# Performance work log

Hardware: AMD Instinct MI355X
Metric: run time of the kernel (lower is better)

The kernel has to match this reference:

```python
import jax, jax.numpy as jnp
import numpy as np

D_MODEL = 1024
NHEAD = 16
HEAD_DIM = D_MODEL // NHEAD
ROPE_BASE = 10000.0


def rope_cos_sin(seq_len, dim, dtype=jnp.float32):
    inv_freq = 1.0 / (ROPE_BASE ** (jnp.arange(0, dim, 2, dtype=jnp.float32) / dim))
    t = jnp.arange(seq_len, dtype=jnp.float32)
    freqs = jnp.einsum('i,j->ij', t, inv_freq)        # [S, dim/2]
    emb = jnp.concatenate([freqs, freqs], axis=-1)    # [S, dim]
    return emb.astype(dtype), jnp.cos(emb).astype(dtype), jnp.sin(emb).astype(dtype)


def rotate_half(x):
    x1, x2 = jnp.split(x, 2, axis=-1)
    return jnp.concatenate([-x2, x1], axis=-1)


def setup_inputs() -> dict:
    key = jax.random.key(0)
    ks = jax.random.split(key, 11)
    B, S, D = 2, 2048, D_MODEL
    std = 1.0 / np.sqrt(D)
    return {
        'query': jax.random.normal(ks[0], (B, S, D), jnp.float32),
        'key_': jax.random.normal(ks[1], (B, S, D), jnp.float32),
        'value': jax.random.normal(ks[2], (B, S, D), jnp.float32),
        'Wq': jax.random.uniform(ks[3], (D, D), jnp.float32, -std, std),
        'bq': jax.random.uniform(ks[4], (D,), jnp.float32, -std, std),
        'Wk': jax.random.uniform(ks[5], (D, D), jnp.float32, -std, std),
        'bk': jax.random.uniform(ks[6], (D,), jnp.float32, -std, std),
        'Wv': jax.random.uniform(ks[7], (D, D), jnp.float32, -std, std),
        'bv': jax.random.uniform(ks[8], (D,), jnp.float32, -std, std),
        'Wo': jax.random.uniform(ks[9], (D, D), jnp.float32, -std, std),
        'bo': jax.random.uniform(ks[10], (D,), jnp.float32, -std, std),
    }


def reference(query, key_, value, Wq, bq, Wk, bk, Wv, bv, Wo, bo):
    B, T, D = query.shape
    S = key_.shape[1]
    H, Hd = NHEAD, HEAD_DIM
    scale = Hd ** -0.5
    # projections (torch Linear: x @ W^T + b), reshape to [B, H, L, Hd]
    q = (query @ Wq.T + bq).reshape(B, T, H, Hd).transpose(0, 2, 1, 3)
    k = (key_ @ Wk.T + bk).reshape(B, S, H, Hd).transpose(0, 2, 1, 3)
    v = (value @ Wv.T + bv).reshape(B, S, H, Hd).transpose(0, 2, 1, 3)
    # RoPE
    _, cos, sin = rope_cos_sin(max(T, S), Hd, query.dtype)
    cos_q, sin_q = cos[:T][None, None], sin[:S][None, None]
    q = q * cos_q + rotate_half(q) * sin_q
    k = k * cos_q + rotate_half(k) * sin_q
    # attention
    scores = jnp.einsum('bhtd,bhsd->bhts', q, k) * scale
    attn = jax.nn.softmax(scores, axis=-1)
    out = jnp.einsum('bhts,bhsd->bhtd', attn, v)
    out = out.transpose(0, 2, 1, 3).reshape(B, T, D)
    return out @ Wo.T + bo
```

## Files before the change

kernel.cpp:

```cpp
#include <hip/hip_runtime.h>
#include <hip/hip_bf16.h>
#include <math.h>

using bf16x8 = __attribute__((ext_vector_type(8))) short;
using f32x4  = __attribute__((ext_vector_type(4))) float;
using f32x16 = __attribute__((ext_vector_type(16))) float;

#define MFMA16(a,b,c) __builtin_amdgcn_mfma_f32_16x16x32_bf16(a,b,c,0,0,0)
#define MFMA32(a,b,c) __builtin_amdgcn_mfma_f32_32x32x16_bf16(a,b,c,0,0,0)

#define GLOAD_LDS16(g, s) __builtin_amdgcn_global_load_lds( \
    (const __attribute__((address_space(1))) unsigned int*)(const void*)(g), \
    (__attribute__((address_space(3))) unsigned int*)(void*)(s), 16, 0, 0)

static __device__ __forceinline__ short f2bf(float f) {
    __hip_bfloat16 h = __float2bfloat16(f);
    return *reinterpret_cast<short*>(&h);
}

static __device__ __forceinline__ int cvtpk(float lo, float hi) {
    int r;
    asm volatile("v_cvt_pk_bf16_f32 %0, %1, %2" : "=v"(r) : "v"(lo), "v"(hi));
    return r;
}

__global__ void prep_cast(const float* q, const float* k, const float* v,
                          const float* wq, const float* wk, const float* wv, const float* wo,
                          short* xq, short* xk, short* xv,
                          short* bwq, short* bwk, short* bwv, short* bwo) {
    const long NBIG = 1L << 20;
    const long NW   = 1L << 18;
    const long total = 3*NBIG + 4*NW;
    for (long i = (long)blockIdx.x*blockDim.x + threadIdx.x; i < total; i += (long)gridDim.x*blockDim.x) {
        const float* src; short* dst; long j = i;
        if (j < NBIG)              { src = q;  dst = xq;  }
        else if ((j -= NBIG) < NBIG) { src = k;  dst = xk;  }
        else if ((j -= NBIG) < NBIG) { src = v;  dst = xv;  }
        else if ((j -= NBIG) < NW)   { src = wq; dst = bwq; }
        else if ((j -= NW) < NW)     { src = wk; dst = bwk; }
        else if ((j -= NW) < NW)     { src = wv; dst = bwv; }
        else { j -= NW;              src = wo; dst = bwo; }
        float4 f = reinterpret_cast<const float4*>(src)[j];
        ushort4 o;
        o.x = (ushort)f2bf(f.x); o.y = (ushort)f2bf(f.y);
        o.z = (ushort)f2bf(f.z); o.w = (ushort)f2bf(f.w);
        reinterpret_cast<ushort4*>(dst)[j] = o;
    }
}

__global__ void rope_table(float* cost, float* sint) {
    int i = blockIdx.x*blockDim.x + threadIdx.x;
    int s = i >> 5, j = i & 31;
    double inv = pow(10000.0, -(double)j / 32.0);
    double a = (double)s * inv;
    cost[i] = (float)cos(a);
    sint[i] = (float)sin(a);
}

__device__ __forceinline__ void gemm_tile(const short* A, const short* B,
                                          int brow, int bcol, short* lds,
                                          f32x4 (&acc)[4][4]) {
    short* Al0 = lds;
    short* Al1 = lds + 4096;
    short* Bl0 = lds + 8192;
    short* Bl1 = lds + 12288;
    const int t = threadIdx.x;
    const int l = t & 63, qi = l & 15, h = l >> 4;
    const int w = t >> 6, wr = w >> 1, wc = w & 1;
    const f32x4 z4 = {0.f, 0.f, 0.f, 0.f};
#pragma unroll
    for (int i = 0; i < 4; ++i)
#pragma unroll
        for (int j = 0; j < 4; ++j) acc[i][j] = z4;

    const int srow = w*32 + (l >> 2);
    const int scol = (l & 3) << 3;
    const short* ga = A + (long)(brow + srow)*1024 + scol;
    const short* gb = B + (long)(bcol + srow)*1024 + scol;
    const int lo = w*32*32;

    GLOAD_LDS16(ga,            Al0 + lo);
    GLOAD_LDS16(ga + 16*1024,  Al0 + lo + 16*32);
    GLOAD_LDS16(gb,            Bl0 + lo);
    GLOAD_LDS16(gb + 16*1024,  Bl0 + lo + 16*32);
    asm volatile("s_waitcnt vmcnt(0)");
    __syncthreads();

    int cur = 0;
    for (int kt = 0; kt < 32; ++kt) {
        if (kt < 31) {
            short* An = cur ? Al0 : Al1;
            short* Bn = cur ? Bl0 : Bl1;
            GLOAD_LDS16(ga + ((kt+1) << 5),            An + lo);
            GLOAD_LDS16(ga + ((kt+1) << 5) + 16*1024,  An + lo + 16*32);
            GLOAD_LDS16(gb + ((kt+1) << 5),            Bn + lo);
            GLOAD_LDS16(gb + ((kt+1) << 5) + 16*1024,  Bn + lo + 16*32);
        }
        const short* Ac = cur ? Al1 : Al0;
        const short* Bc = cur ? Bl1 : Bl0;
        bf16x8 af[4], bfr[4];
#pragma unroll
        for (int mf = 0; mf < 4; ++mf)
            af[mf] = *(const bf16x8*)(Ac + (wr*64 + mf*16 + qi)*32 + h*8);
#pragma unroll
        for (int nf = 0; nf < 4; ++nf)
            bfr[nf] = *(const bf16x8*)(Bc + (wc*64 + nf*16 + qi)*32 + h*8);
        __builtin_amdgcn_s_setprio(1);
#pragma unroll
        for (int mf = 0; mf < 4; ++mf)
#pragma unroll
            for (int nf = 0; nf < 4; ++nf)
                acc[mf][nf] = MFMA16(af[mf], bfr[nf], acc[mf][nf]);
        __builtin_amdgcn_s_setprio(0);
        asm volatile("s_waitcnt vmcnt(0)");
        __syncthreads();
        cur ^= 1;
    }
}

__global__ __launch_bounds__(256, 3)
void gemm_qkv_kernel(const short* xq, const short* xk, const short* xv,
                     const short* wq, const short* wk, const short* wv,
                     const float* biq, const float* bik, const float* biv,
                     short* qo, short* ko, short* vo,
                     const float* cost, const float* sint) {
    __shared__ __align__(16) short lds[16384];
    const int mode = blockIdx.z;
    const short* A    = mode == 0 ? xq  : (mode == 1 ? xk  : xv);
    const short* B    = mode == 0 ? wq  : (mode == 1 ? wk  : wv);
    const float* bias = mode == 0 ? biq : (mode == 1 ? bik : biv);
    const int brow = blockIdx.x * 128, bcol = blockIdx.y * 128;
    f32x4 acc[4][4];
    gemm_tile(A, B, brow, bcol, lds, acc);

    const int t = threadIdx.x;
    const int l = t & 63, qi = l & 15, h = l >> 4;
    const int w = t >> 6, wr = w >> 1, wc = w & 1;
    const int n0 = bcol + wc*64, m0 = brow + wr*64;

    if (mode < 2) {
        short* dst = mode == 0 ? qo : ko;
        const float sc = (mode == 0) ? 0.125f : 1.0f;
#pragma unroll
        for (int nf = 0; nf < 2; ++nf) {
            const int j = nf*16 + qi;
            const float b0 = bias[n0 + nf*16 + qi];
            const float b1 = bias[n0 + (nf+2)*16 + qi];
#pragma unroll
            for (int mf = 0; mf < 4; ++mf) {
#pragma unroll
                for (int r = 0; r < 4; ++r) {
                    int m = m0 + mf*16 + 4*h + r;
                    int s = m & 2047;
                    float c  = cost[s*32 + j];
                    float si = sint[s*32 + j];
                    float x0 = acc[mf][nf  ][r] + b0;
                    float x1 = acc[mf][nf+2][r] + b1;
                    dst[(long)m*1024 + n0 + nf*16 + qi]      = f2bf((x0*c - x1*si) * sc);
                    dst[(long)m*1024 + n0 + (nf+2)*16 + qi]  = f2bf((x1*c + x0*si) * sc);
                }
            }
        }
    } else {
        __syncthreads();
        short* tb = lds + w*4096;
#pragma unroll
        for (int nf = 0; nf < 4; ++nf) {
            const int dl = nf*16 + qi;
            const float bb = bias[n0 + dl];
#pragma unroll
            for (int mf = 0; mf < 4; ++mf) {
#pragma unroll
                for (int r = 0; r < 4; ++r) {
                    const int sl = mf*16 + 4*h + r;
                    *(short*)((char*)tb + (((dl*64 + sl)*2) ^ ((dl & 7) << 4))) =
                        f2bf(acc[mf][nf][r] + bb);
                }
            }
        }
        const int hh2 = n0 >> 6;
        const int bb2 = m0 >> 11;
        const long s0g = (long)(m0 & 2047);
#pragma unroll
        for (int i = 0; i < 8; ++i) {
            const int c = l + (i << 6);
            const int dl = c >> 3, so = (c & 7) << 3;
            int4 vv = *(const int4*)((char*)tb + (((dl*64 + so)*2) ^ ((dl & 7) << 4)));
            *(int4*)(vo + (long)((bb2*16 + hh2)*64 + dl)*2048 + s0g + so) = vv;
        }
    }
}

__global__ __launch_bounds__(256, 3)
void gemm_o_kernel(const short* A, const short* B, const float* bias, float* out) {
    __shared__ __align__(16) short lds[16384];
    const int brow = blockIdx.x * 128, bcol = blockIdx.y * 128;
    f32x4 acc[4][4];
    gemm_tile(A, B, brow, bcol, lds, acc);
    const int t = threadIdx.x;
    const int l = t & 63, qi = l & 15, h = l >> 4;
    const int w = t >> 6, wr = w >> 1, wc = w & 1;
    const int n0 = bcol + wc*64, m0 = brow + wr*64;
#pragma unroll
    for (int nf = 0; nf < 4; ++nf) {
        float bb = bias[n0 + nf*16 + qi];
#pragma unroll
        for (int mf = 0; mf < 4; ++mf) {
#pragma unroll
            for (int r = 0; r < 4; ++r) {
                int m = m0 + mf*16 + 4*h + r;
                out[(long)m*1024 + n0 + nf*16 + qi] = acc[mf][nf][r] + bb;
            }
        }
    }
}

__global__ __launch_bounds__(256, 2)
void attn_kernel(const short* qw, const short* kw, const short* vtw, short* ow) {
    __shared__ __align__(16) short Kl[64*64];
    __shared__ __align__(16) short Vl[64*64];
    const int t = threadIdx.x;
    const int w = t >> 6, l = t & 63;
    const int q5 = l & 31, hi = l >> 5;
    const int b = blockIdx.z, hh = blockIdx.y;
    const long qrow = (long)b*2048 + blockIdx.x*128 + w*32 + q5;

    bf16x8 bqf[4];
#pragma unroll
    for (int s = 0; s < 4; ++s)
        bqf[s] = *(const bf16x8*)(qw + qrow*1024 + hh*64 + s*16 + hi*8);

    f32x16 o0, o1;
#pragma unroll
    for (int r = 0; r < 16; ++r) { o0[r] = 0.f; o1[r] = 0.f; }
    float mrun = -INFINITY, lrun = 0.f;

    const short* Kg = kw  + (long)b*2048*1024 + hh*64;
    const short* Vg = vtw + (long)(b*16 + hh)*64*2048;

    const int r0a = t >> 3,        e0a = (t & 7) << 3;
    const int r0b = (t+256) >> 3,  e0b = ((t+256) & 7) << 3;

    for (int jt = 0; jt < 32; ++jt) {
        __syncthreads();
        {
            int4 ka = *(const int4*)(Kg + (long)(jt*64 + r0a)*1024 + e0a);
            int4 va = *(const int4*)(Vg + (long)r0a*2048 + jt*64 + e0a);
            int4 kb = *(const int4*)(Kg + (long)(jt*64 + r0b)*1024 + e0b);
            int4 vb = *(const int4*)(Vg + (long)r0b*2048 + jt*64 + e0b);
            *(int4*)((char*)Kl + (((r0a*64 + e0a)*2) ^ ((r0a & 7) << 4))) = ka;
            *(int4*)((char*)Vl + (((r0a*64 + e0a)*2) ^ ((r0a & 7) << 4))) = va;
            *(int4*)((char*)Kl + (((r0b*64 + e0b)*2) ^ ((r0b & 7) << 4))) = kb;
            *(int4*)((char*)Vl + (((r0b*64 + e0b)*2) ^ ((r0b & 7) << 4))) = vb;
        }
        __syncthreads();

        f32x16 s0v, s1v;
#pragma unroll
        for (int r = 0; r < 16; ++r) { s0v[r] = 0.f; s1v[r] = 0.f; }
        __builtin_amdgcn_s_setprio(1);
#pragma unroll
        for (int s = 0; s < 4; ++s) {
            const int cb = (s*16 + hi*8) * 2;
            bf16x8 ka0 = *(const bf16x8*)((char*)Kl + (((q5*64*2) + cb) ^ ((q5 & 7) << 4)));
            bf16x8 ka1 = *(const bf16x8*)((char*)Kl + ((((32+q5)*64*2) + cb) ^ ((q5 & 7) << 4)));
            s0v = MFMA32(ka0, bqf[s], s0v);
            s1v = MFMA32(ka1, bqf[s], s1v);
        }
        __builtin_amdgcn_s_setprio(0);

        float tm = -INFINITY;
#pragma unroll
        for (int r = 0; r < 16; ++r) { tm = fmaxf(tm, s0v[r]); tm = fmaxf(tm, s1v[r]); }
        tm = fmaxf(tm, __shfl_xor(tm, 32));
        const float mnew = fmaxf(mrun, tm);
        const float corr = __expf(mrun - mnew);
        float ts = 0.f;
#pragma unroll
        for (int r = 0; r < 16; ++r) {
            s0v[r] = __expf(s0v[r] - mnew);
            s1v[r] = __expf(s1v[r] - mnew);
            ts += s0v[r] + s1v[r];
        }
        ts += __shfl_xor(ts, 32);
        lrun = lrun*corr + ts;
        mrun = mnew;
#pragma unroll
        for (int r = 0; r < 16; ++r) { o0[r] *= corr; o1[r] *= corr; }

        bf16x8 pf[4];
#pragma unroll
        for (int tt = 0; tt < 2; ++tt) {
#pragma unroll
            for (int ss = 0; ss < 2; ++ss) {
                const int base = 8*ss;
                float p0, p1, p2, p3, p4, p5, p6, p7;
                if (tt == 0) {
                    p0=s0v[base+0]; p1=s0v[base+1]; p2=s0v[base+2]; p3=s0v[base+3];
                    p4=s0v[base+4]; p5=s0v[base+5]; p6=s0v[base+6]; p7=s0v[base+7];
                } else {
                    p0=s1v[base+0]; p1=s1v[base+1]; p2=s1v[base+2]; p3=s1v[base+3];
                    p4=s1v[base+4]; p5=s1v[base+5]; p6=s1v[base+6]; p7=s1v[base+7];
                }
                int X0 = cvtpk(p0, p1), Y0 = cvtpk(p2, p3);
                int X1 = cvtpk(p4, p5), Y1 = cvtpk(p6, p7);
                int sx0 = __shfl_xor(X0, 32), sy0 = __shfl_xor(Y0, 32);
                int sx1 = __shfl_xor(X1, 32), sy1 = __shfl_xor(Y1, 32);
                union { int i[4]; bf16x8 v; } u;
                u.i[0] = hi ? sx1 : X0;
                u.i[1] = hi ? sy1 : Y0;
                u.i[2] = hi ? X1  : sx0;
                u.i[3] = hi ? Y1  : sy0;
                pf[2*tt + ss] = u.v;
            }
        }

        __builtin_amdgcn_s_setprio(1);
#pragma unroll
        for (int s4 = 0; s4 < 4; ++s4) {
            const int cb = (s4*16 + hi*8) * 2;
            bf16x8 va0 = *(const bf16x8*)((char*)Vl + (((q5*64*2) + cb) ^ ((q5 & 7) << 4)));
            bf16x8 va1 = *(const bf16x8*)((char*)Vl + ((((32+q5)*64*2) + cb) ^ ((q5 & 7) << 4)));
            o0 = MFMA32(va0, pf[s4], o0);
            o1 = MFMA32(va1, pf[s4], o1);
        }
        __builtin_amdgcn_s_setprio(0);
    }

    const float inv = 1.f / lrun;
    const long obase = qrow*1024 + hh*64;
#pragma unroll
    for (int dt = 0; dt < 2; ++dt) {
#pragma unroll
        for (int j = 0; j < 4; ++j) {
            ushort4 pk;
            if (dt == 0) {
                pk.x = (ushort)f2bf(o0[4*j+0]*inv); pk.y = (ushort)f2bf(o0[4*j+1]*inv);
                pk.z = (ushort)f2bf(o0[4*j+2]*inv); pk.w = (ushort)f2bf(o0[4*j+3]*inv);
            } else {
                pk.x = (ushort)f2bf(o1[4*j+0]*inv); pk.y = (ushort)f2bf(o1[4*j+1]*inv);
                pk.z = (ushort)f2bf(o1[4*j+2]*inv); pk.w = (ushort)f2bf(o1[4*j+3]*inv);
            }
            *(ushort4*)(ow + obase + dt*32 + 8*j + 4*hi) = pk;
        }
    }
}

extern "C" void kernel_launch(void* const* d_in, const int* in_sizes, int n_in,
                              void* d_out, int out_size, void* d_ws, size_t ws_size,
                              hipStream_t stream) {
    const float* query = (const float*)d_in[0];
    const float* key_  = (const float*)d_in[1];
    const float* value = (const float*)d_in[2];
    const float* Wq = (const float*)d_in[3];
    const float* bq = (const float*)d_in[4];
    const float* Wk = (const float*)d_in[5];
    const float* bk = (const float*)d_in[6];
    const float* Wv = (const float*)d_in[7];
    const float* bv = (const float*)d_in[8];
    const float* Wo = (const float*)d_in[9];
    const float* bo = (const float*)d_in[10];
    float* out = (float*)d_out;

    char* ws = (char*)d_ws;
    const size_t MB = 1u << 20;
    short* xq  = (short*)(ws);
    short* xk  = (short*)(ws + 8*MB);
    short* xv  = (short*)(ws + 16*MB);
    short* wqb = (short*)(ws + 24*MB);
    short* wkb = (short*)(ws + 26*MB);
    short* wvb = (short*)(ws + 28*MB);
    short* wob = (short*)(ws + 30*MB);
    short* qws = (short*)(ws + 32*MB);
    short* kws = (short*)(ws + 40*MB);
    short* vtw = (short*)(ws + 48*MB);
    float* cost = (float*)(ws + 56*MB);
    float* sint = (float*)(ws + 56*MB + 2048*32*4);
    short* attn = xq;

    hipLaunchKernelGGL(prep_cast, dim3(2048), dim3(256), 0, stream,
                       query, key_, value, Wq, Wk, Wv, Wo,
                       xq, xk, xv, wqb, wkb, wvb, wob);
    hipLaunchKernelGGL(rope_table, dim3(256), dim3(256), 0, stream, cost, sint);
    hipLaunchKernelGGL(gemm_qkv_kernel, dim3(32, 8, 3), dim3(256), 0, stream,
                       xq, xk, xv, wqb, wkb, wvb, bq, bk, bv,
                       qws, kws, vtw, cost, sint);
    hipLaunchKernelGGL(attn_kernel, dim3(16, 16, 2), dim3(256), 0, stream,
                       qws, kws, vtw, attn);
    hipLaunchKernelGGL(gemm_o_kernel, dim3(32, 8), dim3(256), 0, stream,
                       attn, wob, bo, out);
}
```

Before: 238.6 us.

## Double-buffer K/V tiles in attention and use exp2 with lazy rescaling

The attention loop now prefetches the next K/V tile into registers at the start of each iteration and stores it into a second LDS buffer after the MFMAs, cutting the two barriers per tile to one and overlapping global loads with compute. Softmax switches to exp2, with log2(e) folded into the Q projection scale. The running max is only updated, and the accumulators rescaled, when any lane's new max exceeds the old one by more than 8. This doubles LDS use and keeps prefetched data live in registers. The lazy rescale lets unnormalised values grow up to 2^8, which matters for bf16 P precision.

```diff
diff --git a/kernel.cpp b/kernel.cpp
--- a/kernel.cpp
+++ b/kernel.cpp
@@ -140,7 +140,7 @@
 
     if (mode < 2) {
         short* dst = mode == 0 ? qo : ko;
-        const float sc = (mode == 0) ? 0.125f : 1.0f;
+        const float sc = (mode == 0) ? 0.125f * 1.44269504088896f : 1.0f;
 #pragma unroll
         for (int nf = 0; nf < 2; ++nf) {
             const int j = nf*16 + qi;
@@ -217,8 +217,8 @@
 
 __global__ __launch_bounds__(256, 2)
 void attn_kernel(const short* qw, const short* kw, const short* vtw, short* ow) {
-    __shared__ __align__(16) short Kl[64*64];
-    __shared__ __align__(16) short Vl[64*64];
+    __shared__ __align__(16) short Kl[2][64*64];
+    __shared__ __align__(16) short Vl[2][64*64];
     const int t = threadIdx.x;
     const int w = t >> 6, l = t & 63;
     const int q5 = l & 31, hi = l >> 5;
@@ -240,20 +240,29 @@
 
     const int r0a = t >> 3,        e0a = (t & 7) << 3;
     const int r0b = (t+256) >> 3,  e0b = ((t+256) & 7) << 3;
-
+    const int swa = (((r0a*64 + e0a)*2) ^ ((r0a & 7) << 4));
+    const int swb = (((r0b*64 + e0b)*2) ^ ((r0b & 7) << 4));
+
+    int4 ka = *(const int4*)(Kg + (long)r0a*1024 + e0a);
+    int4 va = *(const int4*)(Vg + (long)r0a*2048 + e0a);
+    int4 kb = *(const int4*)(Kg + (long)r0b*1024 + e0b);
+    int4 vb = *(const int4*)(Vg + (long)r0b*2048 + e0b);
+    *(int4*)((char*)Kl[0] + swa) = ka;
+    *(int4*)((char*)Vl[0] + swa) = va;
+    *(int4*)((char*)Kl[0] + swb) = kb;
+    *(int4*)((char*)Vl[0] + swb) = vb;
+    __syncthreads();
+
+    int cur = 0;
     for (int jt = 0; jt < 32; ++jt) {
-        __syncthreads();
-        {
-            int4 ka = *(const int4*)(Kg + (long)(jt*64 + r0a)*1024 + e0a);
-            int4 va = *(const int4*)(Vg + (long)r0a*2048 + jt*64 + e0a);
-            int4 kb = *(const int4*)(Kg + (long)(jt*64 + r0b)*1024 + e0b);
-            int4 vb = *(const int4*)(Vg + (long)r0b*2048 + jt*64 + e0b);
-            *(int4*)((char*)Kl + (((r0a*64 + e0a)*2) ^ ((r0a & 7) << 4))) = ka;
-            *(int4*)((char*)Vl + (((r0a*64 + e0a)*2) ^ ((r0a & 7) << 4))) = va;
-            *(int4*)((char*)Kl + (((r0b*64 + e0b)*2) ^ ((r0b & 7) << 4))) = kb;
-            *(int4*)((char*)Vl + (((r0b*64 + e0b)*2) ^ ((r0b & 7) << 4))) = vb;
-        }
-        __syncthreads();
+        if (jt < 31) {
+            ka = *(const int4*)(Kg + (long)((jt+1)*64 + r0a)*1024 + e0a);
+            va = *(const int4*)(Vg + (long)r0a*2048 + (jt+1)*64 + e0a);
+            kb = *(const int4*)(Kg + (long)((jt+1)*64 + r0b)*1024 + e0b);
+            vb = *(const int4*)(Vg + (long)r0b*2048 + (jt+1)*64 + e0b);
+        }
+        const short* Kc = Kl[cur];
+        const short* Vc = Vl[cur];
 
         f32x16 s0v, s1v;
 #pragma unroll
@@ -262,8 +271,8 @@
 #pragma unroll
         for (int s = 0; s < 4; ++s) {
             const int cb = (s*16 + hi*8) * 2;
-            bf16x8 ka0 = *(const bf16x8*)((char*)Kl + (((q5*64*2) + cb) ^ ((q5 & 7) << 4)));
-            bf16x8 ka1 = *(const bf16x8*)((char*)Kl + ((((32+q5)*64*2) + cb) ^ ((q5 & 7) << 4)));
+            bf16x8 ka0 = *(const bf16x8*)((const char*)Kc + (((q5*64*2) + cb) ^ ((q5 & 7) << 4)));
+            bf16x8 ka1 = *(const bf16x8*)((const char*)Kc + ((((32+q5)*64*2) + cb) ^ ((q5 & 7) << 4)));
             s0v = MFMA32(ka0, bqf[s], s0v);
             s1v = MFMA32(ka1, bqf[s], s1v);
         }
@@ -273,20 +282,23 @@
 #pragma unroll
         for (int r = 0; r < 16; ++r) { tm = fmaxf(tm, s0v[r]); tm = fmaxf(tm, s1v[r]); }
         tm = fmaxf(tm, __shfl_xor(tm, 32));
-        const float mnew = fmaxf(mrun, tm);
-        const float corr = __expf(mrun - mnew);
+        if (!__all(tm - mrun <= 8.f)) {
+            const float mnew = fmaxf(mrun, tm);
+            const float corr = __builtin_amdgcn_exp2f(mrun - mnew);
+#pragma unroll
+            for (int r = 0; r < 16; ++r) { o0[r] *= corr; o1[r] *= corr; }
+            lrun *= corr;
+            mrun = mnew;
+        }
         float ts = 0.f;
 #pragma unroll
         for (int r = 0; r < 16; ++r) {
-            s0v[r] = __expf(s0v[r] - mnew);
-            s1v[r] = __expf(s1v[r] - mnew);
+            s0v[r] = __builtin_amdgcn_exp2f(s0v[r] - mrun);
+            s1v[r] = __builtin_amdgcn_exp2f(s1v[r] - mrun);
             ts += s0v[r] + s1v[r];
         }
         ts += __shfl_xor(ts, 32);
-        lrun = lrun*corr + ts;
-        mrun = mnew;
-#pragma unroll
-        for (int r = 0; r < 16; ++r) { o0[r] *= corr; o1[r] *= corr; }
+        lrun += ts;
 
         bf16x8 pf[4];
 #pragma unroll
@@ -319,12 +331,23 @@
 #pragma unroll
         for (int s4 = 0; s4 < 4; ++s4) {
             const int cb = (s4*16 + hi*8) * 2;
-            bf16x8 va0 = *(const bf16x8*)((char*)Vl + (((q5*64*2) + cb) ^ ((q5 & 7) << 4)));
-            bf16x8 va1 = *(const bf16x8*)((char*)Vl + ((((32+q5)*64*2) + cb) ^ ((q5 & 7) << 4)));
+            bf16x8 va0 = *(const bf16x8*)((const char*)Vc + (((q5*64*2) + cb) ^ ((q5 & 7) << 4)));
+            bf16x8 va1 = *(const bf16x8*)((const char*)Vc + ((((32+q5)*64*2) + cb) ^ ((q5 & 7) << 4)));
             o0 = MFMA32(va0, pf[s4], o0);
             o1 = MFMA32(va1, pf[s4], o1);
         }
         __builtin_amdgcn_s_setprio(0);
+
+        if (jt < 31) {
+            short* Kn = Kl[cur ^ 1];
+            short* Vn = Vl[cur ^ 1];
+            *(int4*)((char*)Kn + swa) = ka;
+            *(int4*)((char*)Vn + swa) = va;
+            *(int4*)((char*)Kn + swb) = kb;
+            *(int4*)((char*)Vn + swb) = vb;
+        }
+        __syncthreads();
+        cur ^= 1;
     }
 
     const float inv = 1.f / lrun;
```

New measurement: 225.8 us. 1.06x faster.
